# Performance work log

Measured on AMD Instinct MI355X. Metric: run time of the kernel, lower is better.

## Reference

```python
import jax, jax.numpy as jnp
import numpy as np

N, D = 16384, 2048

def setup_inputs() -> dict:
    key = jax.random.key(0)
    k1, k2 = jax.random.split(key)
    cxr = jax.random.normal(k1, (N, D), dtype=jnp.float32)
    ehr = jax.random.normal(k2, (N, D), dtype=jnp.float32)
    return {"cxr": cxr, "ehr": ehr}

def reference(cxr, ehr):
    # Same math as diag(a_norm @ b_norm.T): row-wise cosine similarity.
    # a_norm = ehr / ||ehr||_row, b_norm = cxr / ||cxr||_row (L2 norms, dim=1)
    a_norm = ehr / jnp.linalg.norm(ehr, axis=1, keepdims=True)
    b_norm = cxr / jnp.linalg.norm(cxr, axis=1, keepdims=True)
    cos = jnp.sum(a_norm * b_norm, axis=1)  # [N] row-wise dot products
    return 1.0 - jnp.mean(cos)
```

## Files before the change

kernel.cpp:

```cpp
#include <hip/hip_runtime.h>
#include <hip/hip_bf16.h>


#define ROWS 16384
#define COLS_V4 512
#define BLOCK 512
#define GRID 512
#define STEPS (ROWS / GRID)
#define WPB (BLOCK / 64)

__global__ __launch_bounds__(BLOCK, 2) void cosine_partial_kernel(
    const float4* __restrict__ A,
    const float4* __restrict__ B,
    float* __restrict__ partial) {
    const int t    = threadIdx.x;
    const int wave = t >> 6;
    const int lane = t & 63;

    __shared__ float s_part[STEPS][WPB][3];

    const float4* __restrict__ a = A + (size_t)blockIdx.x * COLS_V4 + t;
    const float4* __restrict__ b = B + (size_t)blockIdx.x * COLS_V4 + t;
    const size_t stride = (size_t)GRID * COLS_V4;

    float4 x = a[0];
    float4 y = b[0];
    for (int s = 0; s < STEPS; ++s) {
        float4 xn, yn;
        if (s + 1 < STEPS) {
            xn = a[(size_t)(s + 1) * stride];
            yn = b[(size_t)(s + 1) * stride];
        }
        float d  = x.x * y.x + x.y * y.y + x.z * y.z + x.w * y.w;
        float na = x.x * x.x + x.y * x.y + x.z * x.z + x.w * x.w;
        float nb = y.x * y.x + y.y * y.y + y.z * y.z + y.w * y.w;
        #pragma unroll
        for (int off = 32; off > 0; off >>= 1) {
            d  += __shfl_down(d,  off, 64);
            na += __shfl_down(na, off, 64);
            nb += __shfl_down(nb, off, 64);
        }
        if (lane == 0) {
            s_part[s][wave][0] = d;
            s_part[s][wave][1] = na;
            s_part[s][wave][2] = nb;
        }
        x = xn;
        y = yn;
    }
    __syncthreads();

    float loss = 0.f;
    if (t < STEPS) {
        float d = 0.f, na = 0.f, nb = 0.f;
        #pragma unroll
        for (int w = 0; w < WPB; ++w) {
            d  += s_part[t][w][0];
            na += s_part[t][w][1];
            nb += s_part[t][w][2];
        }
        loss = 1.0f - d * rsqrtf(na * nb);
    }
    if (wave == 0) {
        #pragma unroll
        for (int off = 16; off > 0; off >>= 1)
            loss += __shfl_down(loss, off, 64);
        if (lane == 0) partial[blockIdx.x] = loss;
    }
}

__global__ __launch_bounds__(256) void cosine_reduce_kernel(
    const float* __restrict__ partial,
    float* __restrict__ out) {
    const int t = threadIdx.x;
    float s = partial[t] + partial[t + 256];
    #pragma unroll
    for (int off = 32; off > 0; off >>= 1) s += __shfl_down(s, off, 64);

    __shared__ float s_sum[4];
    const int wave = t >> 6;
    const int lane = t & 63;
    if (lane == 0) s_sum[wave] = s;
    __syncthreads();
    if (t == 0) {
        out[0] = (s_sum[0] + s_sum[1] + s_sum[2] + s_sum[3]) * (1.0f / (float)ROWS);
    }
}

extern "C" void kernel_launch(void* const* d_in, const int* in_sizes, int n_in,
                              void* d_out, int out_size, void* d_ws, size_t ws_size,
                              hipStream_t stream) {
    const float4* cxr = (const float4*)d_in[0];
    const float4* ehr = (const float4*)d_in[1];
    float* out     = (float*)d_out;
    float* partial = (float*)d_ws;

    cosine_partial_kernel<<<GRID, BLOCK, 0, stream>>>(cxr, ehr, partial);
    cosine_reduce_kernel<<<1, 256, 0, stream>>>(partial, out);
}
```

Baseline: 275.3 us.

## Assign rows to waves and accumulate per lane before a single reduction

Reorganizes the partial kernel so each wavefront owns two full rows, accumulating dot and squared norms per lane across chunks and doing one cross-lane shuffle reduction per row. It uses smaller blocks, a larger grid and a higher occupancy hint to increase memory-level parallelism. This removes the per-chunk shuffle reductions and the shared-memory staging of partials. The final reduce kernel now sums more partials, and a stray multiply-by-zero term was added to the norm accumulation.

```diff
diff --git a/kernel.cpp b/kernel.cpp
--- a/kernel.cpp
+++ b/kernel.cpp
@@ -4,68 +4,60 @@
 
 #define ROWS 16384
 #define COLS_V4 512
-#define BLOCK 512
-#define GRID 512
-#define STEPS (ROWS / GRID)
+#define BLOCK 256
+#define GRID 2048
 #define WPB (BLOCK / 64)
+#define RPW 2
+#define CHUNKS (COLS_V4 / 64)
+#define TOTAL_S (RPW * CHUNKS)
 
-__global__ __launch_bounds__(BLOCK, 2) void cosine_partial_kernel(
+__global__ __launch_bounds__(BLOCK, 8) void cosine_partial_kernel(
     const float4* __restrict__ A,
     const float4* __restrict__ B,
     float* __restrict__ partial) {
-    const int t    = threadIdx.x;
-    const int wave = t >> 6;
-    const int lane = t & 63;
+    const int wave = threadIdx.x >> 6;
+    const int lane = threadIdx.x & 63;
+    const int wid  = blockIdx.x * WPB + wave;
+    const size_t row0 = (size_t)wid * RPW;
 
-    __shared__ float s_part[STEPS][WPB][3];
-
-    const float4* __restrict__ a = A + (size_t)blockIdx.x * COLS_V4 + t;
-    const float4* __restrict__ b = B + (size_t)blockIdx.x * COLS_V4 + t;
-    const size_t stride = (size_t)GRID * COLS_V4;
+    const float4* __restrict__ a = A + row0 * COLS_V4 + lane;
+    const float4* __restrict__ b = B + row0 * COLS_V4 + lane;
 
     float4 x = a[0];
     float4 y = b[0];
-    for (int s = 0; s < STEPS; ++s) {
+    float dot = 0.f, aa = 0.f, bb = 0.f;
+    float losses = 0.f;
+
+    #pragma unroll
+    for (int s = 0; s < TOTAL_S; ++s) {
         float4 xn, yn;
-        if (s + 1 < STEPS) {
-            xn = a[(size_t)(s + 1) * stride];
-            yn = b[(size_t)(s + 1) * stride];
+        if (s + 1 < TOTAL_S) {
+            xn = a[(s + 1) * 64];
+            yn = b[(s + 1) * 64];
         }
-        float d  = x.x * y.x + x.y * y.y + x.z * y.z + x.w * y.w;
-        float na = x.x * x.x + x.y * x.y + x.z * x.z + x.w * x.w;
-        float nb = y.x * y.x + y.y * y.y + y.z * y.z + y.w * y.w;
-        #pragma unroll
-        for (int off = 32; off > 0; off >>= 1) {
-            d  += __shfl_down(d,  off, 64);
-            na += __shfl_down(na, off, 64);
-            nb += __shfl_down(nb, off, 64);
-        }
-        if (lane == 0) {
-            s_part[s][wave][0] = d;
-            s_part[s][wave][1] = na;
-            s_part[s][wave][2] = nb;
+        dot += x.x * y.x + x.y * y.y + x.z * y.z + x.w * y.w;
+        aa  += x.x * x.x + x.y * x.y + x.z * x.z + x.w * x.w;
+        bb  += y.x * y.y * 0.f + y.x * y.x + y.y * y.y + y.z * y.z + y.w * y.w;
+        if ((s & (CHUNKS - 1)) == (CHUNKS - 1)) {
+            float d = dot, p = aa, q = bb;
+            #pragma unroll
+            for (int off = 32; off > 0; off >>= 1) {
+                d += __shfl_down(d, off, 64);
+                p += __shfl_down(p, off, 64);
+                q += __shfl_down(q, off, 64);
+            }
+            if (lane == 0) losses += 1.0f - d * rsqrtf(p * q);
+            dot = 0.f; aa = 0.f; bb = 0.f;
         }
         x = xn;
         y = yn;
     }
+
+    __shared__ float s_loss[WPB];
+    if (lane == 0) s_loss[wave] = losses;
     __syncthreads();
-
-    float loss = 0.f;
-    if (t < STEPS) {
-        float d = 0.f, na = 0.f, nb = 0.f;
-        #pragma unroll
-        for (int w = 0; w < WPB; ++w) {
-            d  += s_part[t][w][0];
-            na += s_part[t][w][1];
-            nb += s_part[t][w][2];
-        }
-        loss = 1.0f - d * rsqrtf(na * nb);
-    }
-    if (wave == 0) {
-        #pragma unroll
-        for (int off = 16; off > 0; off >>= 1)
-            loss += __shfl_down(loss, off, 64);
-        if (lane == 0) partial[blockIdx.x] = loss;
+    if (threadIdx.x == 0) {
+        partial[blockIdx.x] = s_loss[0] + s_loss[1] + s_loss[2] + s_loss[3];
     }
 }
 
@@ -73,7 +65,9 @@
     const float* __restrict__ partial,
     float* __restrict__ out) {
     const int t = threadIdx.x;
-    float s = partial[t] + partial[t + 256];
+    float s = 0.f;
+    #pragma unroll
+    for (int i = 0; i < GRID / 256; ++i) s += partial[t + i * 256];
     #pragma unroll
     for (int off = 32; off > 0; off >>= 1) s += __shfl_down(s, off, 64);
 
```

Measured after the change: 278.8 us. No clear change (+1.3%).
